# Performance work log

Hardware: AMD Instinct MI355X
Metric: run time of the kernel (lower is better)

The kernel has to match this reference:

```python
import jax, jax.numpy as jnp
import numpy as np

# Action space: 3 discrete action types, 8 options each (MultiDiscrete nvec)
ACTION_NUMS = np.array([8, 8, 8])
A_TOTAL = int(ACTION_NUMS.sum())          # 24
START_IDX = np.cumsum([0, *ACTION_NUMS[:-1]])  # [0, 8, 16]
F, N, D = 4096, 64, 256                   # frames, agents(actions per frame), feat_size
HID = 140                                 # fixed in ForwardNet


def setup_inputs() -> dict:
    key = jax.random.key(0)
    ks = jax.random.split(key, 8)
    s = lambda fan_in: 1.0 / np.sqrt(fan_in)
    return {
        "current_feature": jax.random.normal(ks[0], (F, N, D), jnp.float32),
        "next_feature": jax.random.normal(ks[1], (F, N, D), jnp.float32),
        "actions": jax.random.randint(ks[2], (F, 3, N), 0, 8, dtype=jnp.int32),
        "W1": jax.random.normal(ks[3], (D + A_TOTAL, HID), jnp.float32) * s(D + A_TOTAL),
        "b1": jnp.zeros((HID,), jnp.float32),
        "W2": jax.random.normal(ks[4], (HID, D), jnp.float32) * s(HID),
        "b2": jnp.zeros((D,), jnp.float32),
        "Wi": jax.random.normal(ks[5], (2 * D, A_TOTAL), jnp.float32) * s(2 * D),
        "bi": jnp.zeros((A_TOTAL,), jnp.float32),
    }


def actions2onehot(actions):
    # actions: [F, T, N] int. Vectorized replacement for the triple Python loop:
    # each (frame, agent) row gets a 1 at START_IDX[type] + action, per type.
    start = jnp.asarray(START_IDX, actions.dtype)          # [T]
    idx = actions + start[None, :, None]                    # [F, T, N]
    oh = jax.nn.one_hot(idx, A_TOTAL, dtype=jnp.float32)    # [F, T, N, A]
    return oh.sum(axis=1)                                   # [F, N, A] (column ranges disjoint)


def reference(current_feature, next_feature, actions, W1, b1, W2, b2, Wi, bi):
    action_one_hot = actions2onehot(actions)                       # [F, N, 24]
    # Forward dynamics (attn_target != ICM branch)
    fwd_in = jnp.concatenate([current_feature, action_one_hot], axis=2)  # [F, N, 280]
    h = jax.nn.leaky_relu(fwd_in @ W1 + b1, negative_slope=0.1)
    next_feature_pred = h @ W2 + b2                                # [F, N, 256]
    # Inverse dynamics
    inv_in = jnp.concatenate([current_feature, next_feature], axis=2)   # [F, N, 512]
    action_pred = inv_in @ Wi + bi                                 # [F, N, 24] per-type logits concatenated
    return next_feature_pred, action_pred
```

## Files before the change

### kernel.cpp

```cpp
#include <hip/hip_runtime.h>
#include <hip/hip_bf16.h>
#include <stdint.h>


typedef __attribute__((ext_vector_type(8))) short short8;
typedef __attribute__((ext_vector_type(4))) float float4v;

#define MFMA16 __builtin_amdgcn_mfma_f32_16x16x32_bf16

__device__ __align__(16) uint16_t g_wpack[98816];

static __device__ __forceinline__ void gl_lds16(const void* g, void* l) {
    __builtin_amdgcn_global_load_lds(
        (const __attribute__((address_space(1))) unsigned int*)g,
        (__attribute__((address_space(3))) unsigned int*)l, 16, 0, 0);
}

static __device__ __forceinline__ uint16_t f2bf(float f) {
    __hip_bfloat16 h = __float2bfloat16(f);
    return *reinterpret_cast<uint16_t*>(&h);
}

static __device__ __forceinline__ int pk2(float lo, float hi) {
    __hip_bfloat162 b = __float22bfloat162_rn(make_float2(lo, hi));
    int u; __builtin_memcpy(&u, &b, 4); return u;
}

static __device__ __forceinline__ short8 cvt8(float4v x0, float4v x1) {
    union { __hip_bfloat162 b2[4]; short8 s; } u;
    u.b2[0] = __float22bfloat162_rn(make_float2(x0[0], x0[1]));
    u.b2[1] = __float22bfloat162_rn(make_float2(x0[2], x0[3]));
    u.b2[2] = __float22bfloat162_rn(make_float2(x1[0], x1[1]));
    u.b2[3] = __float22bfloat162_rn(make_float2(x1[2], x1[3]));
    return u.s;
}

__global__ __launch_bounds__(256) void pack_weights(
    const float* __restrict__ W1, const float* __restrict__ W2,
    const float* __restrict__ Wi)
{
    int e = blockIdx.x * 256 + threadIdx.x;
    if (e >= 98816) return;
    if (e >= 41472 && e < 82432) {
        int le = e - 41472;
        int i = le & 7, lane = (le >> 3) & 63, frag = le >> 9;
        int kt = frag >> 4, nt = frag & 15;
        int k = kt * 32 + ((i >= 4) ? 16 : 0) + ((lane >> 4) << 2) + (i & 3);
        int n = nt * 16 + (lane & 15);
        float v = (k < 140) ? W2[k * 256 + n] : 0.0f;
        g_wpack[e] = f2bf(v);
        return;
    }
    const float* W; int NT, Kr, Nr, ld, le, base;
    if (e < 41472) { W = W1; NT = 9; Kr = 280; Nr = 140; ld = 140; le = e;         base = 0; }
    else           { W = Wi; NT = 2; Kr = 512; Nr = 24;  ld = 24;  le = e - 82432; base = 82432; }
    int i = le & 7, lane = (le >> 3) & 63, frag = le >> 9;
    int kt = frag / NT, nt = frag - kt * NT;
    int k = kt * 32 + ((lane >> 4) << 3) + i;
    int n = nt * 16 + (lane & 15);
    float v = (k < Kr && n < Nr) ? W[k * ld + n] : 0.0f;
    g_wpack[base + le] = f2bf(v);
}

__global__ __launch_bounds__(512, 4) void icm_main(
    const float* __restrict__ cf, const float* __restrict__ nf,
    const int* __restrict__ act,
    const float* __restrict__ b1, const float* __restrict__ b2,
    const float* __restrict__ bi,
    float* __restrict__ out)
{
    __shared__ char smem[67584];
    char* bufA = smem;
    char* bufB = smem + 33792;

    const int tid  = threadIdx.x;
    const int wave = tid >> 6;
    const int lane = tid & 63;
    const int lhi  = lane >> 4;
    const int llo  = lane & 15;

    const long rowbase = (long)blockIdx.x * 128 + wave * 16;
    const char* gw = (const char*)g_wpack;

    auto stage1 = [&](char* dst, int kt) {
        const char* w1b = gw + kt * 9216;
        const char* wib = gw + 164864 + kt * 2048;
        const int nb = (kt == 8) ? 9216 : 11264;
        #pragma unroll
        for (int k = 0; k < 2; ++k) {
            int b = k * 8192 + wave * 1024;
            if (b < nb) {
                const char* src = (b < 9216) ? (w1b + b) : (wib + (b - 9216));
                gl_lds16(src + lane * 16, dst + b);
            }
        }
    };
    auto stage16 = [&](char* dst, const char* src) {
        #pragma unroll
        for (int k = 0; k < 2; ++k) {
            int b = k * 8192 + wave * 1024;
            gl_lds16(src + b + lane * 16, dst + b);
        }
    };
    auto stage32 = [&](char* dst, const char* src) {
        #pragma unroll
        for (int k = 0; k < 4; ++k) {
            int b = k * 8192 + wave * 1024;
            gl_lds16(src + b + lane * 16, dst + b);
        }
    };

    int i0, i1, i2;
    {
        long r = rowbase + llo;
        long f = r >> 6; int n = (int)(r & 63);
        i0 = act[(f * 3 + 0) * 64 + n];
        i1 = act[(f * 3 + 1) * 64 + n] + 8;
        i2 = act[(f * 3 + 2) * 64 + n] + 16;
    }

    const float4v fz = {0.f, 0.f, 0.f, 0.f};
    float4v acc1[9];
    float4v acc3[2];
    #pragma unroll
    for (int n = 0; n < 9; ++n) acc1[n] = fz;
    acc3[0] = fz; acc3[1] = fz;

    const float* cfb = cf + (rowbase + llo) * 256 + lhi * 8;

    float4v pa0, pa1, pb0, pb1;

    auto g1 = [&](const char* base, int kt) {
        short8 a = (kt & 1) ? cvt8(pb0, pb1) : cvt8(pa0, pa1);
        if (kt <= 5) {
            int o = (kt + 2) * 32;
            if (kt & 1) { pb0 = *(const float4v*)(cfb + o); pb1 = *(const float4v*)(cfb + o + 4); }
            else        { pa0 = *(const float4v*)(cfb + o); pa1 = *(const float4v*)(cfb + o + 4); }
        }
        #pragma unroll
        for (int nt = 0; nt < 9; ++nt) {
            short8 bf = *(const short8*)(base + (nt << 10) + (lane << 4));
            acc1[nt] = MFMA16(bf, a, acc1[nt], 0, 0, 0);
        }
        #pragma unroll
        for (int nt = 0; nt < 2; ++nt) {
            short8 bf = *(const short8*)(base + ((9 + nt) << 10) + (lane << 4));
            acc3[nt] = MFMA16(bf, a, acc3[nt], 0, 0, 0);
        }
    };

    stage1(bufA, 0); stage1(bufA + 11264, 1); stage1(bufA + 22528, 2);
    pa0 = *(const float4v*)(cfb);      pa1 = *(const float4v*)(cfb + 4);
    pb0 = *(const float4v*)(cfb + 32); pb1 = *(const float4v*)(cfb + 36);
    __syncthreads();

    stage1(bufB, 3); stage1(bufB + 11264, 4); stage1(bufB + 22528, 5);
    g1(bufA, 0); g1(bufA + 11264, 1); g1(bufA + 22528, 2);
    __syncthreads();

    stage1(bufA, 6); stage1(bufA + 11264, 7); stage1(bufA + 22528, 8);
    g1(bufB, 3); g1(bufB + 11264, 4); g1(bufB + 22528, 5);
    __syncthreads();

    stage16(bufB, gw + 164864 + 16384);
    g1(bufA, 6); g1(bufA + 11264, 7);
    const float* nfb = nf + (rowbase + llo) * 256 + lhi * 8;
    pa0 = *(const float4v*)(nfb);      pa1 = *(const float4v*)(nfb + 4);
    pb0 = *(const float4v*)(nfb + 32); pb1 = *(const float4v*)(nfb + 36);
    {
        short8 a;
        #pragma unroll
        for (int i = 0; i < 8; ++i) {
            int kk = lhi * 8 + i;
            a[i] = (kk == i0 || kk == i1 || kk == i2) ? (short)0x3F80 : (short)0;
        }
        const char* base = bufA + 22528;
        #pragma unroll
        for (int nt = 0; nt < 9; ++nt) {
            short8 bf = *(const short8*)(base + (nt << 10) + (lane << 4));
            acc1[nt] = MFMA16(bf, a, acc1[nt], 0, 0, 0);
        }
    }
    __syncthreads();

    stage32(bufA, gw + 82944);

    short8 hb[5];
    #pragma unroll
    for (int kt = 0; kt < 5; ++kt) {
        int cLo = 2 * kt * 16 + lhi * 4;
        int cHi = (2 * kt + 1) * 16 + lhi * 4;
        if (cLo > 136) cLo = 136;
        float4v bLo = *(const float4v*)(b1 + cLo);
        float4v bHi = (kt < 4) ? *(const float4v*)(b1 + cHi) : fz;
        union { int d[4]; short8 s; } t;
        float v0 = acc1[2 * kt][0] + bLo[0]; v0 = v0 > 0.f ? v0 : 0.1f * v0;
        float v1 = acc1[2 * kt][1] + bLo[1]; v1 = v1 > 0.f ? v1 : 0.1f * v1;
        float v2 = acc1[2 * kt][2] + bLo[2]; v2 = v2 > 0.f ? v2 : 0.1f * v2;
        float v3 = acc1[2 * kt][3] + bLo[3]; v3 = v3 > 0.f ? v3 : 0.1f * v3;
        t.d[0] = pk2(v0, v1);
        t.d[1] = pk2(v2, v3);
        if (kt < 4) {
            float w0 = acc1[2 * kt + 1][0] + bHi[0]; w0 = w0 > 0.f ? w0 : 0.1f * w0;
            float w1 = acc1[2 * kt + 1][1] + bHi[1]; w1 = w1 > 0.f ? w1 : 0.1f * w1;
            float w2 = acc1[2 * kt + 1][2] + bHi[2]; w2 = w2 > 0.f ? w2 : 0.1f * w2;
            float w3 = acc1[2 * kt + 1][3] + bHi[3]; w3 = w3 > 0.f ? w3 : 0.1f * w3;
            t.d[2] = pk2(w0, w1);
            t.d[3] = pk2(w2, w3);
        } else { t.d[2] = 0; t.d[3] = 0; }
        hb[kt] = t.s;
    }

    #pragma unroll 1
    for (int kt = 0; kt < 8; ++kt) {
        short8 a = (kt & 1) ? cvt8(pb0, pb1) : cvt8(pa0, pa1);
        if (kt <= 5) {
            int o = (kt + 2) * 32;
            if (kt & 1) { pb0 = *(const float4v*)(nfb + o); pb1 = *(const float4v*)(nfb + o + 4); }
            else        { pa0 = *(const float4v*)(nfb + o); pa1 = *(const float4v*)(nfb + o + 4); }
        }
        #pragma unroll
        for (int nt = 0; nt < 2; ++nt) {
            int f = 2 * kt + nt;
            short8 bf = *(const short8*)(bufB + (f << 10) + (lane << 4));
            acc3[nt] = MFMA16(bf, a, acc3[nt], 0, 0, 0);
        }
    }
    float* out2 = out + 67108864L;
    #pragma unroll
    for (int nt = 0; nt < 2; ++nt) {
        if (nt == 0 || lhi < 2) {
            float4v biv = *(const float4v*)(bi + nt * 16 + lhi * 4);
            long row = rowbase + llo;
            float4v v = acc3[nt];
            v[0] += biv[0]; v[1] += biv[1]; v[2] += biv[2]; v[3] += biv[3];
            *(float4v*)(out2 + row * 24 + nt * 16 + lhi * 4) = v;
        }
    }
    __syncthreads();

    float4v acc2[16];
    #pragma unroll
    for (int n = 0; n < 16; ++n) acc2[n] = fz;

    stage32(bufB, gw + 82944 + 32768);
    #pragma unroll
    for (int k = 0; k < 2; ++k) {
        const char* base = bufA + (k << 14);
        #pragma unroll
        for (int n = 0; n < 16; ++n) {
            short8 bf = *(const short8*)(base + (n << 10) + (lane << 4));
            acc2[n] = MFMA16(bf, hb[k], acc2[n], 0, 0, 0);
        }
    }
    __syncthreads();

    stage16(bufA, gw + 82944 + 65536);
    #pragma unroll
    for (int k = 0; k < 2; ++k) {
        const char* base = bufB + (k << 14);
        #pragma unroll
        for (int n = 0; n < 16; ++n) {
            short8 bf = *(const short8*)(base + (n << 10) + (lane << 4));
            acc2[n] = MFMA16(bf, hb[2 + k], acc2[n], 0, 0, 0);
        }
    }
    __syncthreads();

    #pragma unroll
    for (int n = 0; n < 16; ++n) {
        short8 bf = *(const short8*)(bufA + (n << 10) + (lane << 4));
        acc2[n] = MFMA16(bf, hb[4], acc2[n], 0, 0, 0);
    }

    #pragma unroll
    for (int n = 0; n < 16; ++n) {
        float4v b2v = *(const float4v*)(b2 + n * 16 + lhi * 4);
        long row = rowbase + llo;
        float4v v = acc2[n];
        v[0] += b2v[0]; v[1] += b2v[1]; v[2] += b2v[2]; v[3] += b2v[3];
        *(float4v*)(out + row * 256 + n * 16 + lhi * 4) = v;
    }
}

extern "C" void kernel_launch(void* const* d_in, const int* in_sizes, int n_in,
                              void* d_out, int out_size, void* d_ws, size_t ws_size,
                              hipStream_t stream) {
    const float *cf = nullptr, *nf = nullptr, *W1 = nullptr, *b1 = nullptr;
    const float *W2 = nullptr, *b2 = nullptr, *Wi = nullptr, *bi = nullptr;
    const int *ac = nullptr;
    for (int i = 0; i < n_in; ++i) {
        int s = in_sizes[i];
        const void* p = d_in[i];
        switch (s) {
            case 67108864: if (!cf) cf = (const float*)p; else nf = (const float*)p; break;
            case 786432:   ac = (const int*)p;   break;
            case 39200:    W1 = (const float*)p; break;
            case 140:      b1 = (const float*)p; break;
            case 35840:    W2 = (const float*)p; break;
            case 256:      b2 = (const float*)p; break;
            case 12288:    Wi = (const float*)p; break;
            case 24:       bi = (const float*)p; break;
            default: break;
        }
    }
    float* ob = (float*)d_out;

    pack_weights<<<386, 256, 0, stream>>>(W1, W2, Wi);
    icm_main<<<2048, 512, 0, stream>>>(cf, nf, ac, b1, b2, bi, ob);
}
```

Measured before the change: 212.9 us.

## Make blocks persistent with W1/Wi resident in LDS across row chunks

Switches to 256 blocks of 1024 threads that each loop over four 256-row chunks. The W1 and Wi packed weights are loaded into LDS once per block and kept resident, while W2 is double-buffered in 16KB slices per chunk. This removes the repeated per-block restaging of first-layer weights and most of the barriers around it. The trade-off is about 145KB of LDS per block, so only one block fits per CU, and grid-level parallelism drops to 256 blocks, which can hurt latency hiding for the streaming activation loads.

```diff
diff --git a/kernel.cpp b/kernel.cpp
--- a/kernel.cpp
+++ b/kernel.cpp
@@ -62,16 +62,18 @@
     g_wpack[base + le] = f2bf(v);
 }
 
-__global__ __launch_bounds__(512, 4) void icm_main(
+__global__ __launch_bounds__(1024, 4) void icm_main(
     const float* __restrict__ cf, const float* __restrict__ nf,
     const int* __restrict__ act,
     const float* __restrict__ b1, const float* __restrict__ b2,
     const float* __restrict__ bi,
     float* __restrict__ out)
 {
-    __shared__ char smem[67584];
-    char* bufA = smem;
-    char* bufB = smem + 33792;
+    __shared__ __align__(16) char smem[148480];
+    char* W1L  = smem;
+    char* WiL  = smem + 82944;
+    char* wstA = smem + 115712;
+    char* wstB = smem + 132096;
 
     const int tid  = threadIdx.x;
     const int wave = tid >> 6;
@@ -79,207 +81,168 @@
     const int lhi  = lane >> 4;
     const int llo  = lane & 15;
 
-    const long rowbase = (long)blockIdx.x * 128 + wave * 16;
     const char* gw = (const char*)g_wpack;
-
-    auto stage1 = [&](char* dst, int kt) {
-        const char* w1b = gw + kt * 9216;
-        const char* wib = gw + 164864 + kt * 2048;
-        const int nb = (kt == 8) ? 9216 : 11264;
-        #pragma unroll
-        for (int k = 0; k < 2; ++k) {
-            int b = k * 8192 + wave * 1024;
-            if (b < nb) {
-                const char* src = (b < 9216) ? (w1b + b) : (wib + (b - 9216));
-                gl_lds16(src + lane * 16, dst + b);
-            }
-        }
+    const float4v fz = {0.f, 0.f, 0.f, 0.f};
+
+    #pragma unroll
+    for (int j = 0; j < 6; ++j) {
+        int b = j * 16384 + wave * 1024;
+        if (b < 82944) gl_lds16(gw + b + lane * 16, W1L + b);
+    }
+    #pragma unroll
+    for (int j = 0; j < 2; ++j) {
+        int b = j * 16384 + wave * 1024;
+        gl_lds16(gw + 164864 + b + lane * 16, WiL + b);
+    }
+    auto stage16 = [&](char* dst, const char* src) {
+        int b = wave * 1024;
+        gl_lds16(src + b + lane * 16, dst + b);
     };
-    auto stage16 = [&](char* dst, const char* src) {
-        #pragma unroll
-        for (int k = 0; k < 2; ++k) {
-            int b = k * 8192 + wave * 1024;
-            gl_lds16(src + b + lane * 16, dst + b);
-        }
-    };
-    auto stage32 = [&](char* dst, const char* src) {
-        #pragma unroll
-        for (int k = 0; k < 4; ++k) {
-            int b = k * 8192 + wave * 1024;
-            gl_lds16(src + b + lane * 16, dst + b);
-        }
-    };
-
-    int i0, i1, i2;
-    {
-        long r = rowbase + llo;
-        long f = r >> 6; int n = (int)(r & 63);
-        i0 = act[(f * 3 + 0) * 64 + n];
-        i1 = act[(f * 3 + 1) * 64 + n] + 8;
-        i2 = act[(f * 3 + 2) * 64 + n] + 16;
-    }
-
-    const float4v fz = {0.f, 0.f, 0.f, 0.f};
-    float4v acc1[9];
-    float4v acc3[2];
-    #pragma unroll
-    for (int n = 0; n < 9; ++n) acc1[n] = fz;
-    acc3[0] = fz; acc3[1] = fz;
-
-    const float* cfb = cf + (rowbase + llo) * 256 + lhi * 8;
-
-    float4v pa0, pa1, pb0, pb1;
-
-    auto g1 = [&](const char* base, int kt) {
-        short8 a = (kt & 1) ? cvt8(pb0, pb1) : cvt8(pa0, pa1);
-        if (kt <= 5) {
-            int o = (kt + 2) * 32;
-            if (kt & 1) { pb0 = *(const float4v*)(cfb + o); pb1 = *(const float4v*)(cfb + o + 4); }
-            else        { pa0 = *(const float4v*)(cfb + o); pa1 = *(const float4v*)(cfb + o + 4); }
-        }
-        #pragma unroll
-        for (int nt = 0; nt < 9; ++nt) {
-            short8 bf = *(const short8*)(base + (nt << 10) + (lane << 4));
-            acc1[nt] = MFMA16(bf, a, acc1[nt], 0, 0, 0);
-        }
+    __syncthreads();
+
+    #pragma unroll 1
+    for (int c = 0; c < 4; ++c) {
+        const long rowbase = (long)blockIdx.x * 1024 + c * 256 + wave * 16;
+
+        stage16(wstA, gw + 82944);
+
+        int i0, i1, i2;
+        {
+            long r = rowbase + llo;
+            long f = r >> 6; int n = (int)(r & 63);
+            i0 = act[(f * 3 + 0) * 64 + n];
+            i1 = act[(f * 3 + 1) * 64 + n] + 8;
+            i2 = act[(f * 3 + 2) * 64 + n] + 16;
+        }
+
+        float4v acc1[9];
+        float4v acc3[2];
+        #pragma unroll
+        for (int n = 0; n < 9; ++n) acc1[n] = fz;
+        acc3[0] = fz; acc3[1] = fz;
+
+        const float* cfb = cf + (rowbase + llo) * 256 + lhi * 8;
+        float4v pa0, pa1, pb0, pb1;
+
+        pa0 = *(const float4v*)(cfb);      pa1 = *(const float4v*)(cfb + 4);
+        pb0 = *(const float4v*)(cfb + 32); pb1 = *(const float4v*)(cfb + 36);
+        #pragma unroll 1
+        for (int kt = 0; kt < 8; ++kt) {
+            short8 a = (kt & 1) ? cvt8(pb0, pb1) : cvt8(pa0, pa1);
+            if (kt <= 5) {
+                int o = (kt + 2) * 32;
+                if (kt & 1) { pb0 = *(const float4v*)(cfb + o); pb1 = *(const float4v*)(cfb + o + 4); }
+                else        { pa0 = *(const float4v*)(cfb + o); pa1 = *(const float4v*)(cfb + o + 4); }
+            }
+            const char* base = W1L + kt * 9216;
+            #pragma unroll
+            for (int nt = 0; nt < 9; ++nt) {
+                short8 bf = *(const short8*)(base + (nt << 10) + (lane << 4));
+                acc1[nt] = MFMA16(bf, a, acc1[nt], 0, 0, 0);
+            }
+            #pragma unroll
+            for (int nt = 0; nt < 2; ++nt) {
+                short8 bf = *(const short8*)(WiL + (((kt << 1) + nt) << 10) + (lane << 4));
+                acc3[nt] = MFMA16(bf, a, acc3[nt], 0, 0, 0);
+            }
+        }
+        {
+            short8 a;
+            #pragma unroll
+            for (int i = 0; i < 8; ++i) {
+                int kk = lhi * 8 + i;
+                a[i] = (kk == i0 || kk == i1 || kk == i2) ? (short)0x3F80 : (short)0;
+            }
+            const char* base = W1L + 8 * 9216;
+            #pragma unroll
+            for (int nt = 0; nt < 9; ++nt) {
+                short8 bf = *(const short8*)(base + (nt << 10) + (lane << 4));
+                acc1[nt] = MFMA16(bf, a, acc1[nt], 0, 0, 0);
+            }
+        }
+
+        short8 hb[5];
+        #pragma unroll
+        for (int kt = 0; kt < 5; ++kt) {
+            int cLo = 2 * kt * 16 + lhi * 4;
+            int cHi = (2 * kt + 1) * 16 + lhi * 4;
+            if (cLo > 136) cLo = 136;
+            float4v bLo = *(const float4v*)(b1 + cLo);
+            float4v bHi = (kt < 4) ? *(const float4v*)(b1 + cHi) : fz;
+            union { int d[4]; short8 s; } t;
+            float v0 = acc1[2 * kt][0] + bLo[0]; v0 = v0 > 0.f ? v0 : 0.1f * v0;
+            float v1 = acc1[2 * kt][1] + bLo[1]; v1 = v1 > 0.f ? v1 : 0.1f * v1;
+            float v2 = acc1[2 * kt][2] + bLo[2]; v2 = v2 > 0.f ? v2 : 0.1f * v2;
+            float v3 = acc1[2 * kt][3] + bLo[3]; v3 = v3 > 0.f ? v3 : 0.1f * v3;
+            t.d[0] = pk2(v0, v1);
+            t.d[1] = pk2(v2, v3);
+            if (kt < 4) {
+                float w0 = acc1[2 * kt + 1][0] + bHi[0]; w0 = w0 > 0.f ? w0 : 0.1f * w0;
+                float w1 = acc1[2 * kt + 1][1] + bHi[1]; w1 = w1 > 0.f ? w1 : 0.1f * w1;
+                float w2 = acc1[2 * kt + 1][2] + bHi[2]; w2 = w2 > 0.f ? w2 : 0.1f * w2;
+                float w3 = acc1[2 * kt + 1][3] + bHi[3]; w3 = w3 > 0.f ? w3 : 0.1f * w3;
+                t.d[2] = pk2(w0, w1);
+                t.d[3] = pk2(w2, w3);
+            } else { t.d[2] = 0; t.d[3] = 0; }
+            hb[kt] = t.s;
+        }
+
+        const float* nfb = nf + (rowbase + llo) * 256 + lhi * 8;
+        pa0 = *(const float4v*)(nfb);      pa1 = *(const float4v*)(nfb + 4);
+        pb0 = *(const float4v*)(nfb + 32); pb1 = *(const float4v*)(nfb + 36);
+        #pragma unroll 1
+        for (int kt = 0; kt < 8; ++kt) {
+            short8 a = (kt & 1) ? cvt8(pb0, pb1) : cvt8(pa0, pa1);
+            if (kt <= 5) {
+                int o = (kt + 2) * 32;
+                if (kt & 1) { pb0 = *(const float4v*)(nfb + o); pb1 = *(const float4v*)(nfb + o + 4); }
+                else        { pa0 = *(const float4v*)(nfb + o); pa1 = *(const float4v*)(nfb + o + 4); }
+            }
+            #pragma unroll
+            for (int nt = 0; nt < 2; ++nt) {
+                int f = 16 + 2 * kt + nt;
+                short8 bf = *(const short8*)(WiL + (f << 10) + (lane << 4));
+                acc3[nt] = MFMA16(bf, a, acc3[nt], 0, 0, 0);
+            }
+        }
+        float* out2 = out + 67108864L;
         #pragma unroll
         for (int nt = 0; nt < 2; ++nt) {
-            short8 bf = *(const short8*)(base + ((9 + nt) << 10) + (lane << 4));
-            acc3[nt] = MFMA16(bf, a, acc3[nt], 0, 0, 0);
-        }
-    };
-
-    stage1(bufA, 0); stage1(bufA + 11264, 1); stage1(bufA + 22528, 2);
-    pa0 = *(const float4v*)(cfb);      pa1 = *(const float4v*)(cfb + 4);
-    pb0 = *(const float4v*)(cfb + 32); pb1 = *(const float4v*)(cfb + 36);
-    __syncthreads();
-
-    stage1(bufB, 3); stage1(bufB + 11264, 4); stage1(bufB + 22528, 5);
-    g1(bufA, 0); g1(bufA + 11264, 1); g1(bufA + 22528, 2);
-    __syncthreads();
-
-    stage1(bufA, 6); stage1(bufA + 11264, 7); stage1(bufA + 22528, 8);
-    g1(bufB, 3); g1(bufB + 11264, 4); g1(bufB + 22528, 5);
-    __syncthreads();
-
-    stage16(bufB, gw + 164864 + 16384);
-    g1(bufA, 6); g1(bufA + 11264, 7);
-    const float* nfb = nf + (rowbase + llo) * 256 + lhi * 8;
-    pa0 = *(const float4v*)(nfb);      pa1 = *(const float4v*)(nfb + 4);
-    pb0 = *(const float4v*)(nfb + 32); pb1 = *(const float4v*)(nfb + 36);
-    {
-        short8 a;
-        #pragma unroll
-        for (int i = 0; i < 8; ++i) {
-            int kk = lhi * 8 + i;
-            a[i] = (kk == i0 || kk == i1 || kk == i2) ? (short)0x3F80 : (short)0;
-        }
-        const char* base = bufA + 22528;
-        #pragma unroll
-        for (int nt = 0; nt < 9; ++nt) {
-            short8 bf = *(const short8*)(base + (nt << 10) + (lane << 4));
-            acc1[nt] = MFMA16(bf, a, acc1[nt], 0, 0, 0);
-        }
-    }
-    __syncthreads();
-
-    stage32(bufA, gw + 82944);
-
-    short8 hb[5];
-    #pragma unroll
-    for (int kt = 0; kt < 5; ++kt) {
-        int cLo = 2 * kt * 16 + lhi * 4;
-        int cHi = (2 * kt + 1) * 16 + lhi * 4;
-        if (cLo > 136) cLo = 136;
-        float4v bLo = *(const float4v*)(b1 + cLo);
-        float4v bHi = (kt < 4) ? *(const float4v*)(b1 + cHi) : fz;
-        union { int d[4]; short8 s; } t;
-        float v0 = acc1[2 * kt][0] + bLo[0]; v0 = v0 > 0.f ? v0 : 0.1f * v0;
-        float v1 = acc1[2 * kt][1] + bLo[1]; v1 = v1 > 0.f ? v1 : 0.1f * v1;
-        float v2 = acc1[2 * kt][2] + bLo[2]; v2 = v2 > 0.f ? v2 : 0.1f * v2;
-        float v3 = acc1[2 * kt][3] + bLo[3]; v3 = v3 > 0.f ? v3 : 0.1f * v3;
-        t.d[0] = pk2(v0, v1);
-        t.d[1] = pk2(v2, v3);
-        if (kt < 4) {
-            float w0 = acc1[2 * kt + 1][0] + bHi[0]; w0 = w0 > 0.f ? w0 : 0.1f * w0;
-            float w1 = acc1[2 * kt + 1][1] + bHi[1]; w1 = w1 > 0.f ? w1 : 0.1f * w1;
-            float w2 = acc1[2 * kt + 1][2] + bHi[2]; w2 = w2 > 0.f ? w2 : 0.1f * w2;
-            float w3 = acc1[2 * kt + 1][3] + bHi[3]; w3 = w3 > 0.f ? w3 : 0.1f * w3;
-            t.d[2] = pk2(w0, w1);
-            t.d[3] = pk2(w2, w3);
-        } else { t.d[2] = 0; t.d[3] = 0; }
-        hb[kt] = t.s;
-    }
-
-    #pragma unroll 1
-    for (int kt = 0; kt < 8; ++kt) {
-        short8 a = (kt & 1) ? cvt8(pb0, pb1) : cvt8(pa0, pa1);
-        if (kt <= 5) {
-            int o = (kt + 2) * 32;
-            if (kt & 1) { pb0 = *(const float4v*)(nfb + o); pb1 = *(const float4v*)(nfb + o + 4); }
-            else        { pa0 = *(const float4v*)(nfb + o); pa1 = *(const float4v*)(nfb + o + 4); }
-        }
-        #pragma unroll
-        for (int nt = 0; nt < 2; ++nt) {
-            int f = 2 * kt + nt;
-            short8 bf = *(const short8*)(bufB + (f << 10) + (lane << 4));
-            acc3[nt] = MFMA16(bf, a, acc3[nt], 0, 0, 0);
-        }
-    }
-    float* out2 = out + 67108864L;
-    #pragma unroll
-    for (int nt = 0; nt < 2; ++nt) {
-        if (nt == 0 || lhi < 2) {
-            float4v biv = *(const float4v*)(bi + nt * 16 + lhi * 4);
+            if (nt == 0 || lhi < 2) {
+                float4v biv = *(const float4v*)(bi + nt * 16 + lhi * 4);
+                long row = rowbase + llo;
+                float4v v = acc3[nt];
+                v[0] += biv[0]; v[1] += biv[1]; v[2] += biv[2]; v[3] += biv[3];
+                *(float4v*)(out2 + row * 24 + nt * 16 + lhi * 4) = v;
+            }
+        }
+        __syncthreads();
+
+        float4v acc2[16];
+        #pragma unroll
+        for (int n = 0; n < 16; ++n) acc2[n] = fz;
+
+        #pragma unroll 1
+        for (int kt = 0; kt < 5; ++kt) {
+            if (kt < 4)
+                stage16((kt & 1) ? wstA : wstB, gw + 82944 + (kt + 1) * 16384);
+            const char* wb = (kt & 1) ? wstB : wstA;
+            #pragma unroll
+            for (int n = 0; n < 16; ++n) {
+                short8 bf = *(const short8*)(wb + (n << 10) + (lane << 4));
+                acc2[n] = MFMA16(bf, hb[kt], acc2[n], 0, 0, 0);
+            }
+            __syncthreads();
+        }
+
+        #pragma unroll
+        for (int n = 0; n < 16; ++n) {
+            float4v b2v = *(const float4v*)(b2 + n * 16 + lhi * 4);
             long row = rowbase + llo;
-            float4v v = acc3[nt];
-            v[0] += biv[0]; v[1] += biv[1]; v[2] += biv[2]; v[3] += biv[3];
-            *(float4v*)(out2 + row * 24 + nt * 16 + lhi * 4) = v;
-        }
-    }
-    __syncthreads();
-
-    float4v acc2[16];
-    #pragma unroll
-    for (int n = 0; n < 16; ++n) acc2[n] = fz;
-
-    stage32(bufB, gw + 82944 + 32768);
-    #pragma unroll
-    for (int k = 0; k < 2; ++k) {
-        const char* base = bufA + (k << 14);
-        #pragma unroll
-        for (int n = 0; n < 16; ++n) {
-            short8 bf = *(const short8*)(base + (n << 10) + (lane << 4));
-            acc2[n] = MFMA16(bf, hb[k], acc2[n], 0, 0, 0);
-        }
-    }
-    __syncthreads();
-
-    stage16(bufA, gw + 82944 + 65536);
-    #pragma unroll
-    for (int k = 0; k < 2; ++k) {
-        const char* base = bufB + (k << 14);
-        #pragma unroll
-        for (int n = 0; n < 16; ++n) {
-            short8 bf = *(const short8*)(base + (n << 10) + (lane << 4));
-            acc2[n] = MFMA16(bf, hb[2 + k], acc2[n], 0, 0, 0);
-        }
-    }
-    __syncthreads();
-
-    #pragma unroll
-    for (int n = 0; n < 16; ++n) {
-        short8 bf = *(const short8*)(bufA + (n << 10) + (lane << 4));
-        acc2[n] = MFMA16(bf, hb[4], acc2[n], 0, 0, 0);
-    }
-
-    #pragma unroll
-    for (int n = 0; n < 16; ++n) {
-        float4v b2v = *(const float4v*)(b2 + n * 16 + lhi * 4);
-        long row = rowbase + llo;
-        float4v v = acc2[n];
-        v[0] += b2v[0]; v[1] += b2v[1]; v[2] += b2v[2]; v[3] += b2v[3];
-        *(float4v*)(out + row * 256 + n * 16 + lhi * 4) = v;
+            float4v v = acc2[n];
+            v[0] += b2v[0]; v[1] += b2v[1]; v[2] += b2v[2]; v[3] += b2v[3];
+            *(float4v*)(out + row * 256 + n * 16 + lhi * 4) = v;
+        }
     }
 }
 
@@ -307,5 +270,5 @@
     float* ob = (float*)d_out;
 
     pack_weights<<<386, 256, 0, stream>>>(W1, W2, Wi);
-    icm_main<<<2048, 512, 0, stream>>>(cf, nf, ac, b1, b2, bi, ob);
-}
+    icm_main<<<256, 1024, 0, stream>>>(cf, nf, ac, b1, b2, bi, ob);
+}
```

New measurement: 399.4 us. 1.88x slower.
